# Performance work log

Measured on AMD Instinct MI355X. Metric: run time of the kernel, lower is better.

## Reference

```python
import jax, jax.numpy as jnp
import numpy as np

B, N, E = 2, 4096, 768
H = 12
HD = E // H  # 64

def setup_inputs() -> dict:
    key = jax.random.key(0)
    k1, k2, k3, k4, k5 = jax.random.split(key, 5)
    s = 0.02
    return {
        "x": jax.random.normal(k1, (B, N, E), dtype=jnp.float32),
        "w_qkv": jax.random.normal(k2, (3 * E, E), dtype=jnp.float32) * s,
        "b_qkv": jax.random.normal(k3, (3 * E,), dtype=jnp.float32) * s,
        "w_proj": jax.random.normal(k4, (E, E), dtype=jnp.float32) * s,
        "b_proj": jax.random.normal(k5, (E,), dtype=jnp.float32) * s,
    }

def reference(x, w_qkv, b_qkv, w_proj, b_proj):
    b, n, e = x.shape
    hd = e // H
    # fused QKV projection (torch Linear: x @ W.T + b)
    qkv = jnp.einsum('bne,fe->bnf', x, w_qkv) + b_qkv          # [B,N,3E]
    # faithful to torch reshape(B,N,H,3*hd).permute(0,2,1,3).chunk(3,-1)
    qkv = qkv.reshape(b, n, H, 3 * hd).transpose(0, 2, 1, 3)    # [B,H,N,3hd]
    q, k, v = jnp.split(qkv, 3, axis=-1)                        # each [B,H,N,hd]
    attn = jnp.einsum('bhqd,bhkd->bhqk', q, k) / jnp.sqrt(jnp.float32(hd))
    attn = jax.nn.softmax(attn, axis=-1)                        # [B,H,N,N]
    # dropout layers are identity in eval mode
    out = jnp.einsum('bhqk,bhkd->bhqd', attn, v)                # [B,H,N,hd]
    out = out.transpose(0, 2, 1, 3).reshape(b, n, e)            # [B,N,E]
    out = jnp.einsum('bne,fe->bnf', out, w_proj) + b_proj
    return out
```

## Files before the change

kernel.cpp:

```cpp
#include <hip/hip_runtime.h>

typedef unsigned short u16;
typedef __bf16 bf16x8 __attribute__((ext_vector_type(8)));
typedef float f32x4 __attribute__((ext_vector_type(4)));
typedef unsigned short u16x8 __attribute__((ext_vector_type(8)));
typedef unsigned short u16x4 __attribute__((ext_vector_type(4)));

__device__ __forceinline__ u16 f2bf(float f) {
    __bf16 h = (__bf16)f;
    union { __bf16 h; u16 u; } cv; cv.h = h;
    return cv.u;
}

__device__ __forceinline__ f32x4 mfma16(bf16x8 a, bf16x8 b, f32x4 c) {
    return __builtin_amdgcn_mfma_f32_16x16x32_bf16(a, b, c, 0, 0, 0);
}

__device__ __forceinline__ void gll16(const u16* gp, u16* lp) {
    __builtin_amdgcn_global_load_lds(
        (__attribute__((address_space(1))) void*)const_cast<u16*>(gp),
        (__attribute__((address_space(3))) void*)lp,
        16, 0, 0);
}

__global__ __launch_bounds__(256) void cvt_bf16(const float* __restrict__ in,
                                                u16* __restrict__ out) {
    int i = blockIdx.x * 256 + threadIdx.x;
    const float4* p = (const float4*)in;
    float4 a = p[2 * i];
    float4 b = p[2 * i + 1];
    u16x8 r;
    r[0] = f2bf(a.x); r[1] = f2bf(a.y); r[2] = f2bf(a.z); r[3] = f2bf(a.w);
    r[4] = f2bf(b.x); r[5] = f2bf(b.y); r[6] = f2bf(b.z); r[7] = f2bf(b.w);
    *(u16x8*)&out[8 * i] = r;
}

__global__ __launch_bounds__(256) void gemm_qkv(
    const u16* __restrict__ A, const u16* __restrict__ W,
    const float* __restrict__ bias,
    u16* __restrict__ Qg, u16* __restrict__ Kg, u16* __restrict__ Vtg)
{
    __shared__ __attribute__((aligned(16))) u16 As[128 * 32];
    __shared__ __attribute__((aligned(16))) u16 Bs[128 * 32];
    const int tid = threadIdx.x;
    const int lane = tid & 63, wave = tid >> 6;
    const int lo = lane & 15, hi = lane >> 4;
    const int wm = (wave >> 1) * 64, wn = (wave & 1) * 64;
    const int m0 = blockIdx.y * 128, n0 = blockIdx.x * 128;

    f32x4 acc[4][4];
#pragma unroll
    for (int i = 0; i < 4; i++)
#pragma unroll
        for (int j = 0; j < 4; j++) acc[i][j] = f32x4{0.f, 0.f, 0.f, 0.f};

    const int ar = tid >> 2, ac = (tid & 3) * 8;
    const u16* ga = A + (size_t)(m0 + ar) * 768 + ac;
    const u16* gb = W + (size_t)(n0 + ar) * 768 + ac;

    for (int kt = 0; kt < 768; kt += 32) {
        gll16(ga + kt,            &As[tid * 8]);
        gll16(ga + kt + 64 * 768, &As[2048 + tid * 8]);
        gll16(gb + kt,            &Bs[tid * 8]);
        gll16(gb + kt + 64 * 768, &Bs[2048 + tid * 8]);
        __syncthreads();
        bf16x8 af[4], bfr[4];
#pragma unroll
        for (int mi = 0; mi < 4; mi++)
            af[mi] = *(const bf16x8*)&As[(wm + mi * 16 + lo) * 32 + hi * 8];
#pragma unroll
        for (int ni = 0; ni < 4; ni++)
            bfr[ni] = *(const bf16x8*)&Bs[(wn + ni * 16 + lo) * 32 + hi * 8];
#pragma unroll
        for (int mi = 0; mi < 4; mi++)
#pragma unroll
            for (int ni = 0; ni < 4; ni++)
                acc[mi][ni] = mfma16(af[mi], bfr[ni], acc[mi][ni]);
        __syncthreads();
    }

#pragma unroll
    for (int ni = 0; ni < 4; ni++) {
        const int n = n0 + wn + ni * 16 + lo;
        const int h = n / 192;
        const int rem = n - h * 192;
        const int sel = rem >> 6;
        const int d = rem & 63;
        const float bv = bias[n];
#pragma unroll
        for (int mi = 0; mi < 4; mi++) {
#pragma unroll
            for (int r = 0; r < 4; r++) {
                const int m = m0 + wm + mi * 16 + hi * 4 + r;
                const int bb = m >> 12;
                const int q = m & 4095;
                const float v = acc[mi][ni][r] + bv;
                const size_t bh = (size_t)(bb * 12 + h);
                if (sel == 0) {
                    Qg[(bh * 4096 + q) * 64 + d] = f2bf(v * 0.18033688011112042f);
                } else if (sel == 1) {
                    Kg[(bh * 4096 + q) * 64 + (d ^ ((q & 7) * 8))] = f2bf(v);
                } else {
                    Vtg[(bh * 64 + d) * 4096 +
                        ((q & ~63) | ((q & 63) ^ ((d & 7) * 8)))] = f2bf(v);
                }
            }
        }
    }
}

__global__ __launch_bounds__(256, 3) void attn_kernel(
    const u16* __restrict__ Qg, const u16* __restrict__ Kg,
    const u16* __restrict__ Vtg, u16* __restrict__ Ob)
{
    __shared__ __attribute__((aligned(16))) u16 Ks[128 * 64];
    __shared__ __attribute__((aligned(16))) u16 Vt[64 * 128];
    __shared__ __attribute__((aligned(16))) u16 Ps[8][16 * 64];
    const int tid = threadIdx.x;
    const int lane = tid & 63, wave = tid >> 6;
    const int lo = lane & 15, hi = lane >> 4;
    const int qt = blockIdx.x, h = blockIdx.y, b = blockIdx.z;
    const size_t bh = (size_t)(b * 12 + h);
    const int swl = (lo & 7) * 8;

    bf16x8 qf[2][2];
#pragma unroll
    for (int t = 0; t < 2; t++) {
        const int qrow = qt * 128 + wave * 32 + t * 16 + lo;
        const u16* qp = Qg + (bh * 4096 + qrow) * 64 + hi * 8;
        qf[t][0] = *(const bf16x8*)qp;
        qf[t][1] = *(const bf16x8*)(qp + 32);
    }
    f32x4 o[2][4];
#pragma unroll
    for (int t = 0; t < 2; t++)
#pragma unroll
        for (int i = 0; i < 4; i++) o[t][i] = f32x4{0.f, 0.f, 0.f, 0.f};
    float lp[2] = {0.f, 0.f};

    const u16* gk = Kg + (bh * 4096 + (tid >> 3)) * 64 + (tid & 7) * 8;
    const u16* gv = Vtg + (bh * 64 + (tid >> 4)) * 4096 + (tid & 15) * 8;
    const int pofs = lo * 64 + ((hi * 4) ^ swl);

    for (int kt = 0; kt < 4096; kt += 128) {
#pragma unroll
        for (int c = 0; c < 4; c++)
            gll16(gk + (size_t)(kt + c * 32) * 64, &Ks[c * 2048 + tid * 8]);
#pragma unroll
        for (int c = 0; c < 4; c++)
            gll16(gv + kt + (size_t)c * 16 * 4096, &Vt[c * 2048 + tid * 8]);
        __syncthreads();

#pragma unroll
        for (int half = 0; half < 2; half++) {
#pragma unroll
            for (int ni = 0; ni < 4; ni++) {
                const int row = half * 64 + ni * 16 + lo;
                const bf16x8 kf0 = *(const bf16x8*)&Ks[row * 64 + ((hi * 8) ^ swl)];
                const bf16x8 kf1 = *(const bf16x8*)&Ks[row * 64 + ((32 + hi * 8) ^ swl)];
                f32x4 s0 = mfma16(kf0, qf[0][0], f32x4{0.f, 0.f, 0.f, 0.f});
                s0 = mfma16(kf1, qf[0][1], s0);
                f32x4 s1 = mfma16(kf0, qf[1][0], f32x4{0.f, 0.f, 0.f, 0.f});
                s1 = mfma16(kf1, qf[1][1], s1);
                u16x4 w0, w1;
#pragma unroll
                for (int r = 0; r < 4; r++) {
                    const float p = __builtin_amdgcn_exp2f(s0[r]);
                    lp[0] += p; w0[r] = f2bf(p);
                }
#pragma unroll
                for (int r = 0; r < 4; r++) {
                    const float p = __builtin_amdgcn_exp2f(s1[r]);
                    lp[1] += p; w1[r] = f2bf(p);
                }
                *(u16x4*)&Ps[wave * 2 + 0][pofs ^ (ni * 16)] = w0;
                *(u16x4*)&Ps[wave * 2 + 1][pofs ^ (ni * 16)] = w1;
            }
            bf16x8 pf[2][2];
#pragma unroll
            for (int t = 0; t < 2; t++)
#pragma unroll
                for (int p = 0; p < 2; p++)
                    pf[t][p] = *(const bf16x8*)&Ps[wave * 2 + t]
                        [lo * 64 + ((p * 32 + hi * 8) ^ swl)];

#pragma unroll
            for (int di = 0; di < 4; di++) {
                const int base = (di * 16 + lo) * 128 + half * 64;
#pragma unroll
                for (int p = 0; p < 2; p++) {
                    const bf16x8 vt = *(const bf16x8*)
                        &Vt[base + ((p * 32 + hi * 8) ^ swl)];
                    o[0][di] = mfma16(pf[0][p], vt, o[0][di]);
                    o[1][di] = mfma16(pf[1][p], vt, o[1][di]);
                }
            }
        }
        __syncthreads();
    }

#pragma unroll
    for (int t = 0; t < 2; t++) {
        lp[t] += __shfl_xor(lp[t], 16, 64);
        lp[t] += __shfl_xor(lp[t], 32, 64);
    }

#pragma unroll
    for (int t = 0; t < 2; t++) {
#pragma unroll
        for (int r = 0; r < 4; r++) {
            const float rs = __shfl(lp[t], hi * 4 + r, 64);
            const float inv = 1.f / rs;
            const int q = qt * 128 + wave * 32 + t * 16 + hi * 4 + r;
            u16* op = Ob + ((size_t)b * 4096 + q) * 768 + h * 64 + lo;
#pragma unroll
            for (int di = 0; di < 4; di++)
                op[di * 16] = f2bf(o[t][di][r] * inv);
        }
    }
}

__global__ __launch_bounds__(256) void gemm_proj(
    const u16* __restrict__ A, const u16* __restrict__ W,
    const float* __restrict__ bias, float* __restrict__ C)
{
    __shared__ __attribute__((aligned(16))) u16 As[128 * 32];
    __shared__ __attribute__((aligned(16))) u16 Bs[128 * 32];
    const int tid = threadIdx.x;
    const int lane = tid & 63, wave = tid >> 6;
    const int lo = lane & 15, hi = lane >> 4;
    const int wm = (wave >> 1) * 64, wn = (wave & 1) * 64;
    const int m0 = blockIdx.y * 128, n0 = blockIdx.x * 128;

    f32x4 acc[4][4];
#pragma unroll
    for (int i = 0; i < 4; i++)
#pragma unroll
        for (int j = 0; j < 4; j++) acc[i][j] = f32x4{0.f, 0.f, 0.f, 0.f};

    const int ar = tid >> 2, ac = (tid & 3) * 8;
    const u16* ga = A + (size_t)(m0 + ar) * 768 + ac;
    const u16* gb = W + (size_t)(n0 + ar) * 768 + ac;

    for (int kt = 0; kt < 768; kt += 32) {
        gll16(ga + kt,            &As[tid * 8]);
        gll16(ga + kt + 64 * 768, &As[2048 + tid * 8]);
        gll16(gb + kt,            &Bs[tid * 8]);
        gll16(gb + kt + 64 * 768, &Bs[2048 + tid * 8]);
        __syncthreads();
        bf16x8 af[4], bfr[4];
#pragma unroll
        for (int mi = 0; mi < 4; mi++)
            af[mi] = *(const bf16x8*)&As[(wm + mi * 16 + lo) * 32 + hi * 8];
#pragma unroll
        for (int ni = 0; ni < 4; ni++)
            bfr[ni] = *(const bf16x8*)&Bs[(wn + ni * 16 + lo) * 32 + hi * 8];
#pragma unroll
        for (int mi = 0; mi < 4; mi++)
#pragma unroll
            for (int ni = 0; ni < 4; ni++)
                acc[mi][ni] = mfma16(af[mi], bfr[ni], acc[mi][ni]);
        __syncthreads();
    }

#pragma unroll
    for (int ni = 0; ni < 4; ni++) {
        const int n = n0 + wn + ni * 16 + lo;
        const float bv = bias[n];
#pragma unroll
        for (int mi = 0; mi < 4; mi++) {
#pragma unroll
            for (int r = 0; r < 4; r++) {
                const int m = m0 + wm + mi * 16 + hi * 4 + r;
                C[(size_t)m * 768 + n] = acc[mi][ni][r] + bv;
            }
        }
    }
}

extern "C" void kernel_launch(void* const* d_in, const int* in_sizes, int n_in,
                              void* d_out, int out_size, void* d_ws, size_t ws_size,
                              hipStream_t stream)
{
    const float* x      = (const float*)d_in[0];
    const float* w_qkv  = (const float*)d_in[1];
    const float* b_qkv  = (const float*)d_in[2];
    const float* w_proj = (const float*)d_in[3];
    const float* b_proj = (const float*)d_in[4];
    float* out = (float*)d_out;

    u16* ws  = (u16*)d_ws;
    u16* xb  = ws;
    u16* wqb = xb + 6291456;
    u16* wpb = wqb + 1769472;
    u16* Qg  = wpb + 589824;
    u16* Kg  = Qg + 6291456;
    u16* Vtg = Kg + 6291456;
    u16* Ob  = Vtg + 6291456;

    cvt_bf16<<<3072, 256, 0, stream>>>(x, xb);
    cvt_bf16<<<864,  256, 0, stream>>>(w_qkv, wqb);
    cvt_bf16<<<288,  256, 0, stream>>>(w_proj, wpb);
    gemm_qkv<<<dim3(18, 64), 256, 0, stream>>>(xb, wqb, b_qkv, Qg, Kg, Vtg);
    attn_kernel<<<dim3(32, 12, 2), 256, 0, stream>>>(Qg, Kg, Vtg, Ob);
    gemm_proj<<<dim3(6, 64), 256, 0, stream>>>(Ob, wpb, b_proj, out);
}
```

Measured before the change: 279.8 us.

## Load V fragments directly from global memory and merge conversion kernels

The attention kernel no longer stages transposed V tiles in LDS. Each wave now reads its V^T MFMA fragments straight from global memory, which relies on L2 reuse across the four waves. The QKV GEMM therefore writes Vt unswizzled. The three fp32-to-bf16 conversion launches are merged into one kernel that picks its source by block index. This cuts LDS traffic, LDS footprint and launch overhead, at the cost of redundant global/L2 reads of V per wave and exposed load latency inside the loop.

```diff
diff --git a/kernel.cpp b/kernel.cpp
--- a/kernel.cpp
+++ b/kernel.cpp
@@ -23,16 +23,24 @@
         16, 0, 0);
 }
 
-__global__ __launch_bounds__(256) void cvt_bf16(const float* __restrict__ in,
-                                                u16* __restrict__ out) {
-    int i = blockIdx.x * 256 + threadIdx.x;
-    const float4* p = (const float4*)in;
+__global__ __launch_bounds__(256) void cvt_all(
+    const float* __restrict__ x, const float* __restrict__ wq,
+    const float* __restrict__ wp,
+    u16* __restrict__ xb, u16* __restrict__ wqb, u16* __restrict__ wpb)
+{
+    const int blk = blockIdx.x;
+    const float* src; u16* dst; int base;
+    if (blk < 3072)      { src = x;  dst = xb;  base = 0; }
+    else if (blk < 3936) { src = wq; dst = wqb; base = 3072; }
+    else                 { src = wp; dst = wpb; base = 3936; }
+    const int i = (blk - base) * 256 + threadIdx.x;
+    const float4* p = (const float4*)src;
     float4 a = p[2 * i];
     float4 b = p[2 * i + 1];
     u16x8 r;
     r[0] = f2bf(a.x); r[1] = f2bf(a.y); r[2] = f2bf(a.z); r[3] = f2bf(a.w);
     r[4] = f2bf(b.x); r[5] = f2bf(b.y); r[6] = f2bf(b.z); r[7] = f2bf(b.w);
-    *(u16x8*)&out[8 * i] = r;
+    *(u16x8*)&dst[8 * i] = r;
 }
 
 __global__ __launch_bounds__(256) void gemm_qkv(
@@ -101,8 +109,7 @@
                 } else if (sel == 1) {
                     Kg[(bh * 4096 + q) * 64 + (d ^ ((q & 7) * 8))] = f2bf(v);
                 } else {
-                    Vtg[(bh * 64 + d) * 4096 +
-                        ((q & ~63) | ((q & 63) ^ ((d & 7) * 8)))] = f2bf(v);
+                    Vtg[(bh * 64 + d) * 4096 + q] = f2bf(v);
                 }
             }
         }
@@ -114,7 +121,6 @@
     const u16* __restrict__ Vtg, u16* __restrict__ Ob)
 {
     __shared__ __attribute__((aligned(16))) u16 Ks[128 * 64];
-    __shared__ __attribute__((aligned(16))) u16 Vt[64 * 128];
     __shared__ __attribute__((aligned(16))) u16 Ps[8][16 * 64];
     const int tid = threadIdx.x;
     const int lane = tid & 63, wave = tid >> 6;
@@ -139,20 +145,25 @@
     float lp[2] = {0.f, 0.f};
 
     const u16* gk = Kg + (bh * 4096 + (tid >> 3)) * 64 + (tid & 7) * 8;
-    const u16* gv = Vtg + (bh * 64 + (tid >> 4)) * 4096 + (tid & 15) * 8;
+    const u16* Vb = Vtg + bh * 64 * 4096;
     const int pofs = lo * 64 + ((hi * 4) ^ swl);
 
     for (int kt = 0; kt < 4096; kt += 128) {
 #pragma unroll
         for (int c = 0; c < 4; c++)
             gll16(gk + (size_t)(kt + c * 32) * 64, &Ks[c * 2048 + tid * 8]);
-#pragma unroll
-        for (int c = 0; c < 4; c++)
-            gll16(gv + kt + (size_t)c * 16 * 4096, &Vt[c * 2048 + tid * 8]);
         __syncthreads();
 
 #pragma unroll
         for (int half = 0; half < 2; half++) {
+            bf16x8 vf[4][2];
+#pragma unroll
+            for (int di = 0; di < 4; di++) {
+                const u16* vp = Vb + (size_t)(di * 16 + lo) * 4096
+                                + kt + half * 64 + hi * 8;
+                vf[di][0] = *(const bf16x8*)vp;
+                vf[di][1] = *(const bf16x8*)(vp + 32);
+            }
 #pragma unroll
             for (int ni = 0; ni < 4; ni++) {
                 const int row = half * 64 + ni * 16 + lo;
@@ -186,13 +197,10 @@
 
 #pragma unroll
             for (int di = 0; di < 4; di++) {
-                const int base = (di * 16 + lo) * 128 + half * 64;
 #pragma unroll
                 for (int p = 0; p < 2; p++) {
-                    const bf16x8 vt = *(const bf16x8*)
-                        &Vt[base + ((p * 32 + hi * 8) ^ swl)];
-                    o[0][di] = mfma16(pf[0][p], vt, o[0][di]);
-                    o[1][di] = mfma16(pf[1][p], vt, o[1][di]);
+                    o[0][di] = mfma16(pf[0][p], vf[di][p], o[0][di]);
+                    o[1][di] = mfma16(pf[1][p], vf[di][p], o[1][di]);
                 }
             }
         }
@@ -298,9 +306,7 @@
     u16* Vtg = Kg + 6291456;
     u16* Ob  = Vtg + 6291456;
 
-    cvt_bf16<<<3072, 256, 0, stream>>>(x, xb);
-    cvt_bf16<<<864,  256, 0, stream>>>(w_qkv, wqb);
-    cvt_bf16<<<288,  256, 0, stream>>>(w_proj, wpb);
+    cvt_all<<<4224, 256, 0, stream>>>(x, w_qkv, w_proj, xb, wqb, wpb);
     gemm_qkv<<<dim3(18, 64), 256, 0, stream>>>(xb, wqb, b_qkv, Qg, Kg, Vtg);
     attn_kernel<<<dim3(32, 12, 2), 256, 0, stream>>>(Qg, Kg, Vtg, Ob);
     gemm_proj<<<dim3(6, 64), 256, 0, stream>>>(Ob, wpb, b_proj, out);
```

New measurement: 357.7 us. +27.9%, slower.
